# Kernel optimization log

Hardware: AMD Instinct MI355X
Metric: run time of the kernel (lower is better)

Reference implementation:

```python
import jax, jax.numpy as jnp
import numpy as np

EPS = 1e-6  # module epsilon
FG = 1      # foreground_class_idx
MIN_PIX = 10


def setup_inputs() -> dict:
    key = jax.random.key(0)
    B, C, H, W = 32, 2, 1024, 1024
    segmentation_probs = jax.random.normal(key, (B, C, H, W), dtype=jnp.float32)
    return {"segmentation_probs": segmentation_probs}


def reference(segmentation_probs):
    B, C, H, W = segmentation_probs.shape
    N = H * W
    # One object per batch item: foreground argmax mask (torch.nonzero gather
    # replaced by masked reductions over the full pixel grid).
    pred = jnp.argmax(segmentation_probs, axis=1)            # (B, H, W)
    w = (pred == FG).reshape(B, N).astype(segmentation_probs.dtype)  # (B, N) 0/1

    ys, xs = jnp.meshgrid(jnp.arange(H), jnp.arange(W), indexing='ij')
    # torch.nonzero returns (row, col) -> coord0 = y, coord1 = x
    coords = jnp.stack([ys, xs], axis=-1).reshape(N, 2).astype(segmentation_probs.dtype)

    n = w.sum(axis=1)                                        # (B,) pixel counts
    n_safe = jnp.maximum(n, 2.0)
    centroid = (w @ coords) / n_safe[:, None]                # (B, 2)

    cy = coords[None, :, 0] - centroid[:, 0:1]               # (B, N)
    cx = coords[None, :, 1] - centroid[:, 1:2]               # (B, N)

    # torch.cov uses unbiased (n-1) denominator; centered coords have zero mean
    denom = jnp.maximum(n_safe - 1.0, 1.0)
    Syy = (w * cy * cy).sum(axis=1) / denom
    Sxy = (w * cy * cx).sum(axis=1) / denom
    Sxx = (w * cx * cx).sum(axis=1) / denom

    # closed-form inverse of 2x2 (cov + eps*I)
    a = Syy + EPS
    d = Sxx + EPS
    b = Sxy
    det = a * d - b * b
    i00 = d / det
    i11 = a / det
    i01 = -b / det

    # Mahalanobis terms = diag(P Sigma^-1 P^T), computed elementwise (O(N))
    m = cy * cy * i00[:, None] + 2.0 * cy * cx * i01[:, None] + cx * cx * i11[:, None]
    loss_obj = (w * (m - 1.0) ** 2).sum(axis=1) / n_safe     # masked mean per object

    valid = (n >= MIN_PIX).astype(segmentation_probs.dtype)
    cnt = valid.sum()
    total = (valid * loss_obj).sum()
    return jnp.where(cnt > 0, total / jnp.maximum(cnt, 1.0), 0.0)
```

## Files before the change

kernel.cpp:

```cpp
#include <hip/hip_runtime.h>


constexpr int BATCH = 32;
constexpr int H = 1024;
constexpr int W = 1024;
constexpr int NPIX = H * W;
constexpr int NMOM = 15;
constexpr int TPB = 256;
constexpr int WAVES_PER_BLOCK = TPB / 64;
constexpr int BLOCKS_PER_BATCH = 32;
constexpr int WAVES_PER_BATCH = BLOCKS_PER_BATCH * WAVES_PER_BLOCK;
constexpr int ROWS_PER_WAVE = H / WAVES_PER_BATCH;
constexpr int NBLOCKS = BATCH * BLOCKS_PER_BATCH;


__global__ __launch_bounds__(TPB) void esl_moments(
    const float* __restrict__ probs, double* __restrict__ partials) {
  const int b = blockIdx.x >> 5;
  const int blk = blockIdx.x & 31;
  const int lane = threadIdx.x & 63;
  const int wid = threadIdx.x >> 6;
  const int wave_idx = blk * WAVES_PER_BLOCK + wid;
  const int y0 = wave_idx * ROWS_PER_WAVE;

  const float* __restrict__ p0 = probs + (size_t)b * 2 * NPIX;
  const float* __restrict__ p1 = p0 + NPIX;

  const double X = (double)(4 * lane);
  const double X2 = X * X, X3 = X2 * X, X4 = X2 * X2;

  double acc[NMOM];
#pragma unroll
  for (int i = 0; i < NMOM; ++i) acc[i] = 0.0;

  for (int r = 0; r < ROWS_PER_WAVE; ++r) {
    const int y = y0 + r;
    const float4* __restrict__ r0 =
        reinterpret_cast<const float4*>(p0 + (size_t)y * W);
    const float4* __restrict__ r1 =
        reinterpret_cast<const float4*>(p1 + (size_t)y * W);

    float4 av[4], bv[4];
#pragma unroll
    for (int j = 0; j < 4; ++j) av[j] = r0[j * 64 + lane];
#pragma unroll
    for (int j = 0; j < 4; ++j) bv[j] = r1[j * 64 + lane];

    unsigned s0 = 0, s1 = 0, s2 = 0;
    unsigned long long s3 = 0, s4 = 0;
#pragma unroll
    for (int j = 0; j < 4; ++j) {
      const float pa[4] = {av[j].x, av[j].y, av[j].z, av[j].w};
      const float pb[4] = {bv[j].x, bv[j].y, bv[j].z, bv[j].w};
#pragma unroll
      for (int t = 0; t < 4; ++t) {
        const unsigned long long v = (unsigned long long)(256 * j + t);
        const bool m = pb[t] > pa[t];
        s0 += m ? 1u : 0u;
        s1 += m ? (unsigned)v : 0u;
        s2 += m ? (unsigned)(v * v) : 0u;
        s3 += m ? v * v * v : 0ull;
        s4 += m ? v * v * v * v : 0ull;
      }
    }

    const double S0 = s0, S1 = s1, S2 = s2, S3 = (double)s3, S4 = (double)s4;
    const double T0 = S0;
    const double T1 = X * S0 + S1;
    const double T2 = X2 * S0 + 2.0 * X * S1 + S2;
    const double T3 = X3 * S0 + 3.0 * X2 * S1 + 3.0 * X * S2 + S3;
    const double T4 = X4 * S0 + 4.0 * X3 * S1 + 6.0 * X2 * S2 + 4.0 * X * S3 + S4;
    const double Y = (double)y;
    const double Y2 = Y * Y, Y3 = Y2 * Y, Y4 = Y2 * Y2;
    acc[0] += T0;
    acc[1] += Y * T0;
    acc[2] += T1;
    acc[3] += Y2 * T0;
    acc[4] += Y * T1;
    acc[5] += T2;
    acc[6] += Y3 * T0;
    acc[7] += Y2 * T1;
    acc[8] += Y * T2;
    acc[9] += T3;
    acc[10] += Y4 * T0;
    acc[11] += Y3 * T1;
    acc[12] += Y2 * T2;
    acc[13] += Y * T3;
    acc[14] += T4;
  }

  __shared__ double smem[WAVES_PER_BLOCK][NMOM];
#pragma unroll
  for (int i = 0; i < NMOM; ++i) {
    double v = acc[i];
    for (int o = 32; o > 0; o >>= 1) v += __shfl_down(v, o, 64);
    if (lane == 0) smem[wid][i] = v;
  }
  __syncthreads();
  if (threadIdx.x < NMOM) {
    double v = 0.0;
#pragma unroll
    for (int wv = 0; wv < WAVES_PER_BLOCK; ++wv) v += smem[wv][threadIdx.x];
    partials[blockIdx.x * 16 + threadIdx.x] = v;
  }
}

__global__ __launch_bounds__(512) void esl_finalize(
    const double* __restrict__ partials, float* __restrict__ out) {
  __shared__ double M[BATCH][16];
  __shared__ double red[2];
  const int tid = threadIdx.x;
  const int b = tid >> 4;
  const int i = tid & 15;
  if (i < NMOM) {
    double v = 0.0;
#pragma unroll
    for (int k = 0; k < BLOCKS_PER_BATCH; ++k)
      v += partials[(b * BLOCKS_PER_BATCH + k) * 16 + i];
    M[b][i] = v;
  }
  __syncthreads();

  double loss = 0.0, valid = 0.0;
  if (tid < BATCH) {
    const double* m = M[tid];
    const double n = m[0];
    const double n_safe = fmax(n, 2.0);
    const double ay = m[1] / n_safe;
    const double ax = m[2] / n_safe;
    const double ay2 = ay * ay, ay3 = ay2 * ay, ay4 = ay2 * ay2;
    const double ax2 = ax * ax, ax3 = ax2 * ax, ax4 = ax2 * ax2;

    const double C20 = m[3] - 2.0 * ay * m[1] + ay2 * n;
    const double C11 = m[4] - ay * m[2] - ax * m[1] + ay * ax * n;
    const double C02 = m[5] - 2.0 * ax * m[2] + ax2 * n;

    const double denom = fmax(n_safe - 1.0, 1.0);
    const double Syy = C20 / denom, Sxy = C11 / denom, Sxx = C02 / denom;
    const double a = Syy + 1e-6, d = Sxx + 1e-6, bb = Sxy;
    const double det = a * d - bb * bb;
    const double i00 = d / det, i11 = a / det, i01 = -bb / det;

    const double C40 = m[10] - 4.0 * ay * m[6] + 6.0 * ay2 * m[3]
                     - 4.0 * ay3 * m[1] + ay4 * n;
    const double C31 = m[11] - ax * m[6] - 3.0 * ay * m[7] + 3.0 * ay * ax * m[3]
                     + 3.0 * ay2 * m[4] - 3.0 * ay2 * ax * m[1]
                     - ay3 * m[2] + ay3 * ax * n;
    const double C22 = m[12] - 2.0 * ax * m[7] + ax2 * m[3] - 2.0 * ay * m[8]
                     + 4.0 * ay * ax * m[4] - 2.0 * ay * ax2 * m[1]
                     + ay2 * m[5] - 2.0 * ay2 * ax * m[2] + ay2 * ax2 * n;
    const double C13 = m[13] - ay * m[9] - 3.0 * ax * m[8] + 3.0 * ax * ay * m[5]
                     + 3.0 * ax2 * m[4] - 3.0 * ax2 * ay * m[2]
                     - ax3 * m[1] + ax3 * ay * n;
    const double C04 = m[14] - 4.0 * ax * m[9] + 6.0 * ax2 * m[5]
                     - 4.0 * ax3 * m[2] + ax4 * n;

    const double Swm  = i00 * C20 + 2.0 * i01 * C11 + i11 * C02;
    const double Swm2 = i00 * i00 * C40 + 4.0 * i00 * i01 * C31
                      + (2.0 * i00 * i11 + 4.0 * i01 * i01) * C22
                      + 4.0 * i01 * i11 * C13 + i11 * i11 * C04;
    const double loss_obj = (Swm2 - 2.0 * Swm + n) / n_safe;

    if (n >= 10.0) { valid = 1.0; loss = loss_obj; }
  }
  if (tid < 64) {
    for (int o = 32; o > 0; o >>= 1) {
      loss += __shfl_down(loss, o, 64);
      valid += __shfl_down(valid, o, 64);
    }
    if (tid == 0) {
      red[0] = loss; red[1] = valid;
      out[0] = (float)((red[1] > 0.0) ? red[0] / fmax(red[1], 1.0) : 0.0);
    }
  }
}

extern "C" void kernel_launch(void* const* d_in, const int* in_sizes, int n_in,
                              void* d_out, int out_size, void* d_ws, size_t ws_size,
                              hipStream_t stream) {
  const float* probs = (const float*)d_in[0];
  float* out = (float*)d_out;
  double* partials = (double*)d_ws;
  esl_moments<<<NBLOCKS, TPB, 0, stream>>>(probs, partials);
  esl_finalize<<<1, 512, 0, stream>>>(partials, out);
}
```

Before: 57.66 us.

## Double-buffer row loads with nontemporal reads and double blocks per batch

Restructures the per-wave row loop so the next row's loads are issued before the current row's moment computation. This overlaps memory latency with arithmetic. Loads now use nontemporal hints to avoid cache pollution on this streaming read. Blocks per batch double, so each wave handles fewer rows and more waves are in flight, at the cost of more partials for the finalize kernel to sum and higher register use from the two buffers.

```diff
diff --git a/kernel.cpp b/kernel.cpp
--- a/kernel.cpp
+++ b/kernel.cpp
@@ -8,16 +8,71 @@
 constexpr int NMOM = 15;
 constexpr int TPB = 256;
 constexpr int WAVES_PER_BLOCK = TPB / 64;
-constexpr int BLOCKS_PER_BATCH = 32;
+constexpr int BLOCKS_PER_BATCH = 64;
 constexpr int WAVES_PER_BATCH = BLOCKS_PER_BATCH * WAVES_PER_BLOCK;
 constexpr int ROWS_PER_WAVE = H / WAVES_PER_BATCH;
 constexpr int NBLOCKS = BATCH * BLOCKS_PER_BATCH;
 
+typedef float f32x4 __attribute__((ext_vector_type(4)));
+
+
+__device__ __forceinline__ void load_row(const f32x4* __restrict__ r0,
+                                         const f32x4* __restrict__ r1,
+                                         int lane, f32x4* a, f32x4* b) {
+#pragma unroll
+  for (int j = 0; j < 4; ++j) a[j] = __builtin_nontemporal_load(r0 + j * 64 + lane);
+#pragma unroll
+  for (int j = 0; j < 4; ++j) b[j] = __builtin_nontemporal_load(r1 + j * 64 + lane);
+}
+
+__device__ __forceinline__ void compute_row(const f32x4* a, const f32x4* b, int y,
+                                            const double X, const double X2,
+                                            const double X3, const double X4,
+                                            double* acc) {
+  unsigned s0 = 0, s1 = 0, s2 = 0;
+  unsigned long long s3 = 0, s4 = 0;
+#pragma unroll
+  for (int j = 0; j < 4; ++j) {
+#pragma unroll
+    for (int t = 0; t < 4; ++t) {
+      const unsigned long long v = (unsigned long long)(256 * j + t);
+      const bool m = b[j][t] > a[j][t];
+      s0 += m ? 1u : 0u;
+      s1 += m ? (unsigned)v : 0u;
+      s2 += m ? (unsigned)(v * v) : 0u;
+      s3 += m ? v * v * v : 0ull;
+      s4 += m ? v * v * v * v : 0ull;
+    }
+  }
+  const double S0 = s0, S1 = s1, S2 = s2, S3 = (double)s3, S4 = (double)s4;
+  const double T0 = S0;
+  const double T1 = X * S0 + S1;
+  const double T2 = X2 * S0 + 2.0 * X * S1 + S2;
+  const double T3 = X3 * S0 + 3.0 * X2 * S1 + 3.0 * X * S2 + S3;
+  const double T4 = X4 * S0 + 4.0 * X3 * S1 + 6.0 * X2 * S2 + 4.0 * X * S3 + S4;
+  const double Y = (double)y;
+  const double Y2 = Y * Y, Y3 = Y2 * Y, Y4 = Y2 * Y2;
+  acc[0] += T0;
+  acc[1] += Y * T0;
+  acc[2] += T1;
+  acc[3] += Y2 * T0;
+  acc[4] += Y * T1;
+  acc[5] += T2;
+  acc[6] += Y3 * T0;
+  acc[7] += Y2 * T1;
+  acc[8] += Y * T2;
+  acc[9] += T3;
+  acc[10] += Y4 * T0;
+  acc[11] += Y3 * T1;
+  acc[12] += Y2 * T2;
+  acc[13] += Y * T3;
+  acc[14] += T4;
+}
 
 __global__ __launch_bounds__(TPB) void esl_moments(
     const float* __restrict__ probs, double* __restrict__ partials) {
-  const int b = blockIdx.x >> 5;
-  const int blk = blockIdx.x & 31;
+  const int b = blockIdx.x / BLOCKS_PER_BATCH;
+  const int blk = blockIdx.x % BLOCKS_PER_BATCH;
   const int lane = threadIdx.x & 63;
   const int wid = threadIdx.x >> 6;
   const int wave_idx = blk * WAVES_PER_BLOCK + wid;
@@ -33,60 +88,26 @@
 #pragma unroll
   for (int i = 0; i < NMOM; ++i) acc[i] = 0.0;
 
-  for (int r = 0; r < ROWS_PER_WAVE; ++r) {
-    const int y = y0 + r;
-    const float4* __restrict__ r0 =
-        reinterpret_cast<const float4*>(p0 + (size_t)y * W);
-    const float4* __restrict__ r1 =
-        reinterpret_cast<const float4*>(p1 + (size_t)y * W);
-
-    float4 av[4], bv[4];
-#pragma unroll
-    for (int j = 0; j < 4; ++j) av[j] = r0[j * 64 + lane];
-#pragma unroll
-    for (int j = 0; j < 4; ++j) bv[j] = r1[j * 64 + lane];
-
-    unsigned s0 = 0, s1 = 0, s2 = 0;
-    unsigned long long s3 = 0, s4 = 0;
-#pragma unroll
-    for (int j = 0; j < 4; ++j) {
-      const float pa[4] = {av[j].x, av[j].y, av[j].z, av[j].w};
-      const float pb[4] = {bv[j].x, bv[j].y, bv[j].z, bv[j].w};
-#pragma unroll
-      for (int t = 0; t < 4; ++t) {
-        const unsigned long long v = (unsigned long long)(256 * j + t);
-        const bool m = pb[t] > pa[t];
-        s0 += m ? 1u : 0u;
-        s1 += m ? (unsigned)v : 0u;
-        s2 += m ? (unsigned)(v * v) : 0u;
-        s3 += m ? v * v * v : 0ull;
-        s4 += m ? v * v * v * v : 0ull;
-      }
-    }
-
-    const double S0 = s0, S1 = s1, S2 = s2, S3 = (double)s3, S4 = (double)s4;
-    const double T0 = S0;
-    const double T1 = X * S0 + S1;
-    const double T2 = X2 * S0 + 2.0 * X * S1 + S2;
-    const double T3 = X3 * S0 + 3.0 * X2 * S1 + 3.0 * X * S2 + S3;
-    const double T4 = X4 * S0 + 4.0 * X3 * S1 + 6.0 * X2 * S2 + 4.0 * X * S3 + S4;
-    const double Y = (double)y;
-    const double Y2 = Y * Y, Y3 = Y2 * Y, Y4 = Y2 * Y2;
-    acc[0] += T0;
-    acc[1] += Y * T0;
-    acc[2] += T1;
-    acc[3] += Y2 * T0;
-    acc[4] += Y * T1;
-    acc[5] += T2;
-    acc[6] += Y3 * T0;
-    acc[7] += Y2 * T1;
-    acc[8] += Y * T2;
-    acc[9] += T3;
-    acc[10] += Y4 * T0;
-    acc[11] += Y3 * T1;
-    acc[12] += Y2 * T2;
-    acc[13] += Y * T3;
-    acc[14] += T4;
+  f32x4 a0[4], b0[4], a1[4], b1[4];
+  {
+    const int y = y0;
+    load_row(reinterpret_cast<const f32x4*>(p0 + (size_t)y * W),
+             reinterpret_cast<const f32x4*>(p1 + (size_t)y * W), lane, a0, b0);
+  }
+#pragma unroll
+  for (int r = 0; r < ROWS_PER_WAVE; r += 2) {
+    if (r + 1 < ROWS_PER_WAVE) {
+      const int y = y0 + r + 1;
+      load_row(reinterpret_cast<const f32x4*>(p0 + (size_t)y * W),
+               reinterpret_cast<const f32x4*>(p1 + (size_t)y * W), lane, a1, b1);
+    }
+    compute_row(a0, b0, y0 + r, X, X2, X3, X4, acc);
+    if (r + 2 < ROWS_PER_WAVE) {
+      const int y = y0 + r + 2;
+      load_row(reinterpret_cast<const f32x4*>(p0 + (size_t)y * W),
+               reinterpret_cast<const f32x4*>(p1 + (size_t)y * W), lane, a0, b0);
+    }
+    if (r + 1 < ROWS_PER_WAVE) compute_row(a1, b1, y0 + r + 1, X, X2, X3, X4, acc);
   }
 
   __shared__ double smem[WAVES_PER_BLOCK][NMOM];
```

Result: faster. 56.12 us (-2.7%).
